# Kernel tuning notes

Measured on AMD Instinct MI355X. Metric: run time of the kernel, lower is better.

## Reference

```python
import jax, jax.numpy as jnp
import numpy as np

D_MODEL = 2048
N_HEAD = 32
N_KV_HEAD = 8
HEAD_DIM = D_MODEL // N_HEAD  # 64
N_REP = N_HEAD // N_KV_HEAD   # 4
B, T = 2, 2048


def setup_inputs() -> dict:
    key = jax.random.key(0)
    ks = jax.random.split(key, 5)
    s = 0.02
    return {
        "x": jax.random.normal(ks[0], (B, T, D_MODEL), dtype=jnp.float32),
        "Wq": jax.random.normal(ks[1], (D_MODEL, N_HEAD * HEAD_DIM), dtype=jnp.float32) * s,
        "Wk": jax.random.normal(ks[2], (D_MODEL, N_KV_HEAD * HEAD_DIM), dtype=jnp.float32) * s,
        "Wv": jax.random.normal(ks[3], (D_MODEL, N_KV_HEAD * HEAD_DIM), dtype=jnp.float32) * s,
        "Wo": jax.random.normal(ks[4], (N_HEAD * HEAD_DIM, D_MODEL), dtype=jnp.float32) * s,
        "mask": 1,
    }


def _rope_tables(t_len, dim, dtype):
    inv_freq = 1.0 / (10000.0 ** (jnp.arange(0, dim, 2, dtype=jnp.float32) / dim))
    freqs = jnp.arange(t_len, dtype=jnp.float32)[:, None] * inv_freq[None, :]  # [T, dim/2]
    return jnp.cos(freqs).astype(dtype), jnp.sin(freqs).astype(dtype)


def _apply_rope(x, cos, sin):
    # x: [B, H, T, D]; cos/sin: [T, D/2]; half-concat layout as in source
    x1, x2 = x[..., ::2], x[..., 1::2]
    return jnp.concatenate([x1 * cos - x2 * sin, x1 * sin + x2 * cos], axis=-1)


def reference(x, Wq, Wk, Wv, Wo, mask):
    b, t, c = x.shape
    q = (x @ Wq).reshape(b, t, N_HEAD, HEAD_DIM).transpose(0, 2, 1, 3)      # [B,H,T,D]
    k = (x @ Wk).reshape(b, t, N_KV_HEAD, HEAD_DIM).transpose(0, 2, 1, 3)   # [B,Hkv,T,D]
    v = (x @ Wv).reshape(b, t, N_KV_HEAD, HEAD_DIM).transpose(0, 2, 1, 3)
    cos, sin = _rope_tables(t, HEAD_DIM, x.dtype)
    q = _apply_rope(q, cos, sin)
    k = _apply_rope(k, cos, sin)
    k = jnp.repeat(k, N_REP, axis=1)  # [B,H,T,D]
    v = jnp.repeat(v, N_REP, axis=1)
    scale = 1.0 / np.sqrt(HEAD_DIM)
    scores = jnp.einsum('bhtd,bhsd->bhts', q, k) * scale  # [B,H,T,T]
    if mask:
        causal = jnp.tril(jnp.ones((t, t), dtype=bool))
        scores = jnp.where(causal, scores, jnp.float32(-jnp.inf).astype(scores.dtype))
    weights = jax.nn.softmax(scores, axis=-1)
    out = jnp.einsum('bhts,bhsd->bhtd', weights, v)        # [B,H,T,D]
    out = out.transpose(0, 2, 1, 3).reshape(b, t, c)
    return out @ Wo
```

## Files before the change

kernel.cpp:

```cpp
#include <hip/hip_runtime.h>
#include <stdint.h>

#define D_MODEL 2048
#define N_HEAD 32
#define N_KV_HEAD 8
#define HEAD_DIM 64
#define BATCH 2
#define SEQ 2048
#define ROWS (BATCH*SEQ)
#define QKV_N 3072
#define SCL2F 0.18033688011112042f

typedef __attribute__((ext_vector_type(4))) float f32x4;
typedef __attribute__((ext_vector_type(8))) short bf16x8;

__device__ __forceinline__ float bflo(unsigned u){ return __uint_as_float(u << 16); }
__device__ __forceinline__ float bfhi(unsigned u){ return __uint_as_float(u & 0xFFFF0000u); }
__device__ __forceinline__ unsigned f2bf(float f){
  unsigned u = __float_as_uint(f);
  u += 0x7FFFu + ((u >> 16) & 1u);
  return u >> 16;
}
__device__ __forceinline__ unsigned cvtpk(float a, float b){
  unsigned r;
  asm("v_cvt_pk_bf16_f32 %0, %1, %2" : "=v"(r) : "v"(a), "v"(b));
  return r;
}

__device__ __forceinline__ void async_copy16(const void* g, void* lds){
  __builtin_amdgcn_global_load_lds(
      (const __attribute__((address_space(1))) void*)g,
      (__attribute__((address_space(3))) void*)lds, 16, 0, 0);
}

__global__ __launch_bounds__(256) void k_prep(const float* __restrict__ x,
                                              const float* __restrict__ Wq,
                                              const float* __restrict__ Wk,
                                              const float* __restrict__ Wv,
                                              const float* __restrict__ Wo,
                                              unsigned short* __restrict__ xb,
                                              unsigned short* __restrict__ Wqkvt,
                                              unsigned short* __restrict__ Wot,
                                              float* __restrict__ ct,
                                              float* __restrict__ st){
  __shared__ float tile[64][65];
  const int bid = blockIdx.x;
  const int tid = threadIdx.x;
  if (bid < 8192) {
    int i = bid*256 + tid;
    float4 v = ((const float4*)x)[i];
    unsigned lo = f2bf(v.x) | (f2bf(v.y) << 16);
    unsigned hi = f2bf(v.z) | (f2bf(v.w) << 16);
    ((uint2*)xb)[i] = make_uint2(lo, hi);
    return;
  }
  if (bid < 10752) {
    const int rel0 = bid - 8192;
    const float* W; unsigned short* Wt; int N; int rel;
    if (rel0 < 1024)      { W = Wq; Wt = Wqkvt;                         N = 2048; rel = rel0; }
    else if (rel0 < 1280) { W = Wk; Wt = Wqkvt + (size_t)2048*D_MODEL;  N = 512;  rel = rel0 - 1024; }
    else if (rel0 < 1536) { W = Wv; Wt = Wqkvt + (size_t)2560*D_MODEL;  N = 512;  rel = rel0 - 1280; }
    else                  { W = Wo; Wt = Wot;                           N = 2048; rel = rel0 - 1536; }
    const int ntn = N >> 6;
    const int tk = rel / ntn, tn = rel % ntn;
    #pragma unroll
    for (int i = 0; i < 4; ++i) {
      int idx4 = tid + 256*i;
      int r = idx4 >> 4;
      int c4 = idx4 & 15;
      float4 v = *(const float4*)(W + (size_t)(tk*64 + r)*N + tn*64 + c4*4);
      tile[r][c4*4+0] = v.x; tile[r][c4*4+1] = v.y;
      tile[r][c4*4+2] = v.z; tile[r][c4*4+3] = v.w;
    }
    __syncthreads();
    #pragma unroll
    for (int i = 0; i < 8; ++i) {
      int o2 = tid + 256*i;
      int n  = o2 >> 5;
      int k2 = o2 & 31;
      unsigned lo = f2bf(tile[k2*2+0][n]);
      unsigned hi = f2bf(tile[k2*2+1][n]);
      *(unsigned*)(Wt + (size_t)(tn*64 + n)*D_MODEL + tk*64 + k2*2) = lo | (hi << 16);
    }
    return;
  }
  {
    int gid = (bid - 10752)*256 + tid;
    int t = gid >> 5, d = gid & 31;
    float inv = exp2f(-13.287712379549449f * ((float)d * (1.0f/32.0f)));
    float a = (float)t * inv;
    ct[gid] = cosf(a);
    st[gid] = sinf(a);
  }
}

__global__ __launch_bounds__(256) void k_rope_apply(unsigned short* __restrict__ X,
                                                    const float* __restrict__ ct,
                                                    const float* __restrict__ st,
                                                    int nheads, int stride, float scale){
  int gid = blockIdx.x*256 + threadIdx.x;
  int row = gid / nheads;
  int h = gid - row*nheads;
  int t = row & (SEQ-1);
  unsigned* p = (unsigned*)(X + (size_t)row*stride + h*HEAD_DIM);
  float o1[32], o2[32];
  #pragma unroll
  for (int d = 0; d < 32; ++d) {
    unsigned u = p[d];
    float x1 = bflo(u), x2 = bfhi(u);
    float c = ct[t*32+d], s = st[t*32+d];
    o1[d] = (x1*c - x2*s)*scale;
    o2[d] = (x1*s + x2*c)*scale;
  }
  #pragma unroll
  for (int i = 0; i < 16; ++i) {
    p[i]    = f2bf(o1[2*i]) | (f2bf(o1[2*i+1]) << 16);
    p[16+i] = f2bf(o2[2*i]) | (f2bf(o2[2*i+1]) << 16);
  }
}

template<typename OUT_T>
__global__ __launch_bounds__(256) void k_gemm_bt(const unsigned short* __restrict__ A,
                                                 const unsigned short* __restrict__ Bt,
                                                 OUT_T* __restrict__ C,
                                                 int M, int N, int K){
  __shared__ unsigned short As[128*32];
  __shared__ unsigned short Bs[128*32];
  const int nbn = N >> 7;
  const int bswz = ((int)blockIdx.x & 7)*((int)gridDim.x >> 3) + ((int)blockIdx.x >> 3);
  const int bm = bswz / nbn, bn = bswz % nbn;
  const int m0 = bm << 7, n0 = bn << 7;
  const int tid = threadIdx.x;
  const int wid = tid >> 6, lane = tid & 63;
  const int wr = wid >> 1, wc = wid & 1;

  f32x4 acc[4][4] = {};

  const int ldr = lane >> 2;
  const int ldc = (lane & 3) * 8;
  const int fr  = lane & 15;
  const int fk  = (lane >> 4) * 8;

  for (int k0 = 0; k0 < K; k0 += 32) {
    #pragma unroll
    for (int i = 0; i < 2; ++i) {
      int chunk = wid*2 + i;
      int row = chunk*16 + ldr;
      async_copy16(A  + (size_t)(m0+row)*K + k0 + ldc, (void*)(As + chunk*512));
      async_copy16(Bt + (size_t)(n0+row)*K + k0 + ldc, (void*)(Bs + chunk*512));
    }
    __syncthreads();
    bf16x8 a[4], b[4];
    #pragma unroll
    for (int m = 0; m < 4; ++m) a[m] = *(const bf16x8*)(As + (wr*64 + m*16 + fr)*32 + fk);
    #pragma unroll
    for (int n = 0; n < 4; ++n) b[n] = *(const bf16x8*)(Bs + (wc*64 + n*16 + fr)*32 + fk);
    #pragma unroll
    for (int m = 0; m < 4; ++m)
      #pragma unroll
      for (int n = 0; n < 4; ++n)
        acc[m][n] = __builtin_amdgcn_mfma_f32_16x16x32_bf16(a[m], b[n], acc[m][n], 0, 0, 0);
    __syncthreads();
  }

  const int crow = (lane >> 4) * 4, ccol = lane & 15;
  #pragma unroll
  for (int m = 0; m < 4; ++m){
    #pragma unroll
    for (int n = 0; n < 4; ++n){
      size_t base = (size_t)(m0 + wr*64 + m*16 + crow)*N + (n0 + wc*64 + n*16 + ccol);
      #pragma unroll
      for (int j = 0; j < 4; ++j){
        float v = acc[m][n][j];
        if constexpr (sizeof(OUT_T) == 2)
          ((unsigned short*)C)[base + (size_t)j*N] = (unsigned short)f2bf(v);
        else
          ((float*)C)[base + (size_t)j*N] = v;
      }
    }
  }
}

__global__ __launch_bounds__(256) void k_transpose_v(const unsigned short* __restrict__ Vsrc,
                                                     unsigned short* __restrict__ Vt, int stride){
  __shared__ __align__(16) unsigned short t[64*64];
  const int bk = blockIdx.x >> 5;
  const int st = blockIdx.x & 31;
  const int b = bk >> 3, kvh = bk & 7;
  const int tid = threadIdx.x;
  #pragma unroll
  for (int it = 0; it < 2; ++it) {
    int i = tid + 256*it;
    int s = i >> 3, c = i & 7;
    uint4 v = *(const uint4*)(Vsrc + (size_t)(b*SEQ + st*64 + s)*stride + kvh*HEAD_DIM + c*8);
    *(uint4*)(t + s*64 + ((c ^ (s&7))*8)) = v;
  }
  __syncthreads();
  const int d = tid & 63;
  const int w = tid >> 6;
  #pragma unroll
  for (int it = 0; it < 2; ++it) {
    int seg = w + it*4;
    unsigned short tmp[8];
    #pragma unroll
    for (int k = 0; k < 8; ++k) {
      int s = seg*8 + k;
      tmp[k] = t[s*64 + (((d>>3) ^ (s&7))*8) + (d&7)];
    }
    *(uint4*)(Vt + ((size_t)bk*64 + d)*SEQ + st*64 + seg*8) = *(uint4*)tmp;
  }
}

__global__ __launch_bounds__(256) void k_attn_mfma(const unsigned short* __restrict__ Q,
                                                   const unsigned short* __restrict__ Kb,
                                                   const unsigned short* __restrict__ Vt,
                                                   unsigned short* __restrict__ O,
                                                   const int* __restrict__ maskp,
                                                   const float* __restrict__ ct,
                                                   const float* __restrict__ st){
  __shared__ __align__(16) char smem[32768];
  char* Vsm = smem + 16384;
  const int orig = blockIdx.x;
  const int bid = (orig & 7)*128 + (orig >> 3);
  const int jj = bid & 15;
  const int h  = (bid >> 4) & 31;
  const int b  = bid >> 9;
  const int kvh = h >> 2;
  const int tid = threadIdx.x;
  const int wid = tid >> 6, lane = tid & 63;
  const int q_ = lane & 15, g = lane >> 4;
  char* Psm = smem + 24576 + wid*2048;
  const bool causal = (maskp[0] != 0);

  bf16x8 onesf;
  #pragma unroll
  for (int e = 0; e < 8; ++e) onesf[e] = (short)0x3F80;

  auto stageK = [&](int tile, int bufbase){
    const int s0s = tile*64;
    #pragma unroll
    for (int it = 0; it < 2; ++it) {
      int i = (wid*2+it)*64 + lane;
      int s = i >> 3, c = i & 7;
      async_copy16(Kb + (size_t)(b*SEQ + s0s + s)*QKV_N + kvh*HEAD_DIM + ((c ^ (s&7))*8),
                   smem + bufbase + (wid*2+it)*1024);
    }
  };
  auto stageV = [&](int tile){
    const int s0s = tile*64;
    #pragma unroll
    for (int it = 0; it < 2; ++it) {
      int i = (wid*2+it)*64 + lane;
      int s = i >> 3, c = i & 7;
      async_copy16(Vt + ((size_t)(b*N_KV_HEAD + kvh)*HEAD_DIM + s)*SEQ + s0s + ((c ^ (s&7))*8),
                   Vsm + (wid*2+it)*1024);
    }
  };

  for (int pass = 0; pass < 2; ++pass) {
    const int qt = pass ? jj : (31 - jj);
    const int q0 = qt*64;
    const int qg = q0 + 16*wid + q_;
    const int nt = causal ? (qt+1) : (SEQ/64);

    bf16x8 qf0, qf1;
    {
      const int trow = qg;
      const unsigned short* qsrc = Q + (size_t)(b*SEQ + trow)*QKV_N + h*HEAD_DIM + g*16;
      union { bf16x8 h; unsigned u[4]; } xa, xb;
      xa.h = *(const bf16x8*)(qsrc);
      xb.h = *(const bf16x8*)(qsrc + 8);
      const float4* cp = (const float4*)(ct + trow*32 + g*8);
      const float4* sp = (const float4*)(st + trow*32 + g*8);
      float4 c0 = cp[0], c1 = cp[1];
      float4 s0 = sp[0], s1 = sp[1];
      float cc[8] = {c0.x,c0.y,c0.z,c0.w,c1.x,c1.y,c1.z,c1.w};
      float ss[8] = {s0.x,s0.y,s0.z,s0.w,s1.x,s1.y,s1.z,s1.w};
      float e0[8], e1[8];
      #pragma unroll
      for (int e = 0; e < 8; ++e) {
        unsigned u = (e < 4) ? xa.u[e] : xb.u[e-4];
        float x1 = bflo(u), x2 = bfhi(u);
        float cs = cc[e]*SCL2F, sn = ss[e]*SCL2F;
        e0[e] = x1*cs - x2*sn;
        e1[e] = x1*sn + x2*cs;
      }
      union { unsigned u[4]; bf16x8 h; } p0, p1;
      #pragma unroll
      for (int m = 0; m < 4; ++m) {
        p0.u[m] = cvtpk(e0[2*m], e0[2*m+1]);
        p1.u[m] = cvtpk(e1[2*m], e1[2*m+1]);
      }
      qf0 = p0.h; qf1 = p1.h;
    }

    f32x4 acc[4] = {};
    f32x4 accl = {};
    float mrun = -1e30f;

    stageK(0, 0);
    stageV(0);
    asm volatile("s_waitcnt vmcnt(0)" ::: "memory");
    __syncthreads();

    for (int t = 0; t < nt; ++t) {
      const int s0 = t*64;
      const int cur = t & 1;
      const char* Kbuf = smem + cur*8192;

      if (t+1 < nt) stageK(t+1, (cur^1)*8192);

      f32x4 sa[4];
      __builtin_amdgcn_s_setprio(1);
      #pragma unroll
      for (int f = 0; f < 4; ++f) {
        const char* kb = Kbuf + (16*f + q_)*128;
        bf16x8 a0 = *(const bf16x8*)(kb + ((g ^ (q_&7))*16));
        bf16x8 a1 = *(const bf16x8*)(kb + (((g+4) ^ (q_&7))*16));
        f32x4 z = {};
        z = __builtin_amdgcn_mfma_f32_16x16x32_bf16(a0, qf0, z, 0, 0, 0);
        z = __builtin_amdgcn_mfma_f32_16x16x32_bf16(a1, qf1, z, 0, 0, 0);
        sa[f] = z;
      }
      __builtin_amdgcn_s_setprio(0);

      const bool domask = causal && (t == qt);
      float x[4][4];
      float cm[4];
      #pragma unroll
      for (int f = 0; f < 4; ++f) {
        #pragma unroll
        for (int r = 0; r < 4; ++r) {
          float v = sa[f][r];
          if (domask && (s0 + 16*f + 4*g + r > qg)) v = -3.0e38f;
          x[f][r] = v;
        }
        cm[f] = fmaxf(fmaxf(x[f][0], x[f][1]), fmaxf(x[f][2], x[f][3]));
      }
      float cmax = fmaxf(fmaxf(cm[0], cm[1]), fmaxf(cm[2], cm[3]));
      cmax = fmaxf(cmax, __shfl_xor(cmax, 16));
      cmax = fmaxf(cmax, __shfl_xor(cmax, 32));
      if (!__all(cmax <= mrun + 8.0f)) {
        float mnew = fmaxf(mrun, cmax);
        float r2 = exp2f(mrun - mnew);
        #pragma unroll
        for (int m = 0; m < 4; ++m) {
          acc[m][0] *= r2; acc[m][1] *= r2; acc[m][2] *= r2; acc[m][3] *= r2;
        }
        accl[0] *= r2; accl[1] *= r2; accl[2] *= r2; accl[3] *= r2;
        mrun = mnew;
      }
      #pragma unroll
      for (int f = 0; f < 4; ++f) {
        float e0 = exp2f(x[f][0] - mrun);
        float e1 = exp2f(x[f][1] - mrun);
        float e2 = exp2f(x[f][2] - mrun);
        float e3 = exp2f(x[f][3] - mrun);
        uint2 w = { cvtpk(e0, e1), cvtpk(e2, e3) };
        int byteo = q_*128 + (((2*f + (g>>1)) ^ (q_&7))*16) + (g&1)*8;
        *(uint2*)(Psm + byteo) = w;
      }

      asm volatile("s_waitcnt vmcnt(0)" ::: "memory");
      __syncthreads();

      __builtin_amdgcn_s_setprio(1);
      #pragma unroll
      for (int kh = 0; kh < 2; ++kh) {
        bf16x8 pb = *(const bf16x8*)(Psm + q_*128 + (((g + 4*kh) ^ (q_&7))*16));
        accl = __builtin_amdgcn_mfma_f32_16x16x32_bf16(onesf, pb, accl, 0, 0, 0);
        #pragma unroll
        for (int m = 0; m < 4; ++m) {
          bf16x8 va = *(const bf16x8*)(Vsm + (16*m + q_)*128 + (((g + 4*kh) ^ (q_&7))*16));
          acc[m] = __builtin_amdgcn_mfma_f32_16x16x32_bf16(va, pb, acc[m], 0, 0, 0);
        }
      }
      __builtin_amdgcn_s_setprio(0);

      __syncthreads();
      if (t+1 < nt) stageV(t+1);
    }

    float inv = 1.0f / accl[0];
    #pragma unroll
    for (int m = 0; m < 4; ++m) {
      uint2 w = { cvtpk(acc[m][0]*inv, acc[m][1]*inv), cvtpk(acc[m][2]*inv, acc[m][3]*inv) };
      int byteo = q_*128 + (((2*m + (g>>1)) ^ (q_&7))*16) + (g&1)*8;
      *(uint2*)(Psm + byteo) = w;
    }
    #pragma unroll
    for (int cc = 0; cc < 2; ++cc) {
      int row = lane >> 2;
      int ch = (lane & 3)*2 + cc;
      uint4 v = *(const uint4*)(Psm + row*128 + ((ch ^ (row&7))*16));
      *(uint4*)(O + (size_t)(b*SEQ + q0 + 16*wid + row)*D_MODEL + h*HEAD_DIM + ch*8) = v;
    }
  }
}

extern "C" void kernel_launch(void* const* d_in, const int* in_sizes, int n_in,
                              void* d_out, int out_size, void* d_ws, size_t ws_size,
                              hipStream_t stream){
  const float* x  = (const float*)d_in[0];
  const float* Wq = (const float*)d_in[1];
  const float* Wk = (const float*)d_in[2];
  const float* Wv = (const float*)d_in[3];
  const float* Wo = (const float*)d_in[4];
  const int* maskp = (const int*)d_in[5];
  float* out = (float*)d_out;

  char* ws = (char*)d_ws;
  unsigned short* xb    = (unsigned short*)(ws);
  unsigned short* AO    = (unsigned short*)(ws);
  unsigned short* Wqkvt = (unsigned short*)(ws + 16777216);
  unsigned short* Vt    = (unsigned short*)(ws + 16777216);
  unsigned short* Wot   = (unsigned short*)(ws + 29360128);
  unsigned short* QKVb  = (unsigned short*)(ws + 37748736);
  float* ct = (float*)(ws + 62914560);
  float* st = (float*)(ws + 63176704);

  k_prep<<<11008, 256, 0, stream>>>(x, Wq, Wk, Wv, Wo, xb, Wqkvt, Wot, ct, st);

  k_gemm_bt<unsigned short><<<(4096/128)*(QKV_N/128), 256, 0, stream>>>(xb, Wqkvt, QKVb, 4096, QKV_N, 2048);

  k_rope_apply<<<ROWS*N_KV_HEAD/256, 256, 0, stream>>>(QKVb + 2048, ct, st, N_KV_HEAD, QKV_N, 1.0f);

  k_transpose_v<<<BATCH*N_KV_HEAD*(SEQ/64), 256, 0, stream>>>(QKVb + 2560, Vt, QKV_N);

  k_attn_mfma<<<BATCH*N_HEAD*16, 256, 0, stream>>>(QKVb, QKVb + 2048, Vt, AO, maskp, ct, st);

  k_gemm_bt<float><<<(4096/128)*(2048/128), 256, 0, stream>>>(AO, Wot, out, 4096, 2048, 2048);
}
```

Before: 240.5 us.

## Merge K-rope and V-transpose kernels; double-buffer K and V together in attention

```diff
diff --git a/kernel.cpp b/kernel.cpp
--- a/kernel.cpp
+++ b/kernel.cpp
@@ -94,28 +94,59 @@
   }
 }
 
-__global__ __launch_bounds__(256) void k_rope_apply(unsigned short* __restrict__ X,
-                                                    const float* __restrict__ ct,
-                                                    const float* __restrict__ st,
-                                                    int nheads, int stride, float scale){
-  int gid = blockIdx.x*256 + threadIdx.x;
-  int row = gid / nheads;
-  int h = gid - row*nheads;
-  int t = row & (SEQ-1);
-  unsigned* p = (unsigned*)(X + (size_t)row*stride + h*HEAD_DIM);
-  float o1[32], o2[32];
+__global__ __launch_bounds__(256) void k_kv_prep(unsigned short* __restrict__ QKVb,
+                                                 unsigned short* __restrict__ Vt,
+                                                 const float* __restrict__ ct,
+                                                 const float* __restrict__ st){
+  __shared__ __align__(16) unsigned short tl[64*64];
+  const int bid = blockIdx.x;
+  const int tid = threadIdx.x;
+  if (bid < 128) {
+    int gid = bid*256 + tid;
+    int row = gid >> 3;
+    int h = gid & 7;
+    int t = row & (SEQ-1);
+    unsigned* p = (unsigned*)(QKVb + (size_t)row*QKV_N + 2048 + h*HEAD_DIM);
+    float o1[32], o2[32];
+    #pragma unroll
+    for (int d = 0; d < 32; ++d) {
+      unsigned u = p[d];
+      float x1 = bflo(u), x2 = bfhi(u);
+      float c = ct[t*32+d], s = st[t*32+d];
+      o1[d] = x1*c - x2*s;
+      o2[d] = x1*s + x2*c;
+    }
+    #pragma unroll
+    for (int i = 0; i < 16; ++i) {
+      p[i]    = f2bf(o1[2*i]) | (f2bf(o1[2*i+1]) << 16);
+      p[16+i] = f2bf(o2[2*i]) | (f2bf(o2[2*i+1]) << 16);
+    }
+    return;
+  }
+  const int rel = bid - 128;
+  const int bk = rel >> 5;
+  const int stt = rel & 31;
+  const int b = bk >> 3, kvh = bk & 7;
   #pragma unroll
-  for (int d = 0; d < 32; ++d) {
-    unsigned u = p[d];
-    float x1 = bflo(u), x2 = bfhi(u);
-    float c = ct[t*32+d], s = st[t*32+d];
-    o1[d] = (x1*c - x2*s)*scale;
-    o2[d] = (x1*s + x2*c)*scale;
-  }
+  for (int it = 0; it < 2; ++it) {
+    int i = tid + 256*it;
+    int s = i >> 3, c = i & 7;
+    uint4 v = *(const uint4*)(QKVb + (size_t)(b*SEQ + stt*64 + s)*QKV_N + 2560 + kvh*HEAD_DIM + c*8);
+    *(uint4*)(tl + s*64 + ((c ^ (s&7))*8)) = v;
+  }
+  __syncthreads();
+  const int d = tid & 63;
+  const int w = tid >> 6;
   #pragma unroll
-  for (int i = 0; i < 16; ++i) {
-    p[i]    = f2bf(o1[2*i]) | (f2bf(o1[2*i+1]) << 16);
-    p[16+i] = f2bf(o2[2*i]) | (f2bf(o2[2*i+1]) << 16);
+  for (int it = 0; it < 2; ++it) {
+    int seg = w + it*4;
+    unsigned short tmp[8];
+    #pragma unroll
+    for (int k = 0; k < 8; ++k) {
+      int s = seg*8 + k;
+      tmp[k] = tl[s*64 + (((d>>3) ^ (s&7))*8) + (d&7)];
+    }
+    *(uint4*)(Vt + ((size_t)bk*64 + d)*SEQ + stt*64 + seg*8) = *(uint4*)tmp;
   }
 }
 
@@ -181,36 +212,6 @@
   }
 }
 
-__global__ __launch_bounds__(256) void k_transpose_v(const unsigned short* __restrict__ Vsrc,
-                                                     unsigned short* __restrict__ Vt, int stride){
-  __shared__ __align__(16) unsigned short t[64*64];
-  const int bk = blockIdx.x >> 5;
-  const int st = blockIdx.x & 31;
-  const int b = bk >> 3, kvh = bk & 7;
-  const int tid = threadIdx.x;
-  #pragma unroll
-  for (int it = 0; it < 2; ++it) {
-    int i = tid + 256*it;
-    int s = i >> 3, c = i & 7;
-    uint4 v = *(const uint4*)(Vsrc + (size_t)(b*SEQ + st*64 + s)*stride + kvh*HEAD_DIM + c*8);
-    *(uint4*)(t + s*64 + ((c ^ (s&7))*8)) = v;
-  }
-  __syncthreads();
-  const int d = tid & 63;
-  const int w = tid >> 6;
-  #pragma unroll
-  for (int it = 0; it < 2; ++it) {
-    int seg = w + it*4;
-    unsigned short tmp[8];
-    #pragma unroll
-    for (int k = 0; k < 8; ++k) {
-      int s = seg*8 + k;
-      tmp[k] = t[s*64 + (((d>>3) ^ (s&7))*8) + (d&7)];
-    }
-    *(uint4*)(Vt + ((size_t)bk*64 + d)*SEQ + st*64 + seg*8) = *(uint4*)tmp;
-  }
-}
-
 __global__ __launch_bounds__(256) void k_attn_mfma(const unsigned short* __restrict__ Q,
                                                    const unsigned short* __restrict__ Kb,
                                                    const unsigned short* __restrict__ Vt,
@@ -218,8 +219,7 @@
                                                    const int* __restrict__ maskp,
                                                    const float* __restrict__ ct,
                                                    const float* __restrict__ st){
-  __shared__ __align__(16) char smem[32768];
-  char* Vsm = smem + 16384;
+  __shared__ __align__(16) char smem[40960];
   const int orig = blockIdx.x;
   const int bid = (orig & 7)*128 + (orig >> 3);
   const int jj = bid & 15;
@@ -229,14 +229,14 @@
   const int tid = threadIdx.x;
   const int wid = tid >> 6, lane = tid & 63;
   const int q_ = lane & 15, g = lane >> 4;
-  char* Psm = smem + 24576 + wid*2048;
+  char* Psm = smem + 32768 + wid*2048;
   const bool causal = (maskp[0] != 0);
 
   bf16x8 onesf;
   #pragma unroll
   for (int e = 0; e < 8; ++e) onesf[e] = (short)0x3F80;
 
-  auto stageK = [&](int tile, int bufbase){
+  auto stage = [&](int tile, int bufbase){
     const int s0s = tile*64;
     #pragma unroll
     for (int it = 0; it < 2; ++it) {
@@ -244,16 +244,8 @@
       int s = i >> 3, c = i & 7;
       async_copy16(Kb + (size_t)(b*SEQ + s0s + s)*QKV_N + kvh*HEAD_DIM + ((c ^ (s&7))*8),
                    smem + bufbase + (wid*2+it)*1024);
-    }
-  };
-  auto stageV = [&](int tile){
-    const int s0s = tile*64;
-    #pragma unroll
-    for (int it = 0; it < 2; ++it) {
-      int i = (wid*2+it)*64 + lane;
-      int s = i >> 3, c = i & 7;
       async_copy16(Vt + ((size_t)(b*N_KV_HEAD + kvh)*HEAD_DIM + s)*SEQ + s0s + ((c ^ (s&7))*8),
-                   Vsm + (wid*2+it)*1024);
+                   smem + bufbase + 8192 + (wid*2+it)*1024);
     }
   };
 
@@ -298,17 +290,19 @@
     f32x4 accl = {};
     float mrun = -1e30f;
 
-    stageK(0, 0);
-    stageV(0);
-    asm volatile("s_waitcnt vmcnt(0)" ::: "memory");
     __syncthreads();
+    stage(0, 0);
 
     for (int t = 0; t < nt; ++t) {
       const int s0 = t*64;
       const int cur = t & 1;
-      const char* Kbuf = smem + cur*8192;
-
-      if (t+1 < nt) stageK(t+1, (cur^1)*8192);
+
+      asm volatile("s_waitcnt vmcnt(0)" ::: "memory");
+      __syncthreads();
+      if (t+1 < nt) stage(t+1, (cur^1)*16384);
+
+      const char* Kbuf = smem + cur*16384;
+      const char* Vbuf = Kbuf + 8192;
 
       f32x4 sa[4];
       __builtin_amdgcn_s_setprio(1);
@@ -361,9 +355,6 @@
         *(uint2*)(Psm + byteo) = w;
       }
 
-      asm volatile("s_waitcnt vmcnt(0)" ::: "memory");
-      __syncthreads();
-
       __builtin_amdgcn_s_setprio(1);
       #pragma unroll
       for (int kh = 0; kh < 2; ++kh) {
@@ -371,14 +362,11 @@
         accl = __builtin_amdgcn_mfma_f32_16x16x32_bf16(onesf, pb, accl, 0, 0, 0);
         #pragma unroll
         for (int m = 0; m < 4; ++m) {
-          bf16x8 va = *(const bf16x8*)(Vsm + (16*m + q_)*128 + (((g + 4*kh) ^ (q_&7))*16));
+          bf16x8 va = *(const bf16x8*)(Vbuf + (16*m + q_)*128 + (((g + 4*kh) ^ (q_&7))*16));
           acc[m] = __builtin_amdgcn_mfma_f32_16x16x32_bf16(va, pb, acc[m], 0, 0, 0);
         }
       }
       __builtin_amdgcn_s_setprio(0);
-
-      __syncthreads();
-      if (t+1 < nt) stageV(t+1);
     }
 
     float inv = 1.0f / accl[0];
@@ -423,9 +411,7 @@
 
   k_gemm_bt<unsigned short><<<(4096/128)*(QKV_N/128), 256, 0, stream>>>(xb, Wqkvt, QKVb, 4096, QKV_N, 2048);
 
-  k_rope_apply<<<ROWS*N_KV_HEAD/256, 256, 0, stream>>>(QKVb + 2048, ct, st, N_KV_HEAD, QKV_N, 1.0f);
-
-  k_transpose_v<<<BATCH*N_KV_HEAD*(SEQ/64), 256, 0, stream>>>(QKVb + 2560, Vt, QKV_N);
+  k_kv_prep<<<1152, 256, 0, stream>>>(QKVb, Vt, ct, st);
 
   k_attn_mfma<<<BATCH*N_HEAD*16, 256, 0, stream>>>(QKVb, QKVb + 2048, Vt, AO, maskp, ct, st);
 
```

After: 241.4 us. Within noise of the previous version (+0.4%).
